# Optimization experiments

Measured on AMD Instinct MI355X. Metric: run time of the kernel, lower is better.

## Reference

```python
import jax, jax.numpy as jnp
import numpy as np
import math

N_EXP = 8
TOP_K = 2
CAPACITY_FACTOR = 1.25


def _capacity(num_tokens):
    cap = math.floor(TOP_K * CAPACITY_FACTOR * num_tokens / N_EXP)
    cap += cap % 2  # round up to even, as in nanoMoE
    return int(cap)


def setup_inputs() -> dict:
    key = jax.random.key(0)
    k1, k2, k3, k4 = jax.random.split(key, 4)
    B, C, d = 4, 1024, 1024
    x = jax.random.normal(k1, (B, C, d), dtype=jnp.float32)
    w_g = jax.random.normal(k2, (d, N_EXP), dtype=jnp.float32) * 0.02
    c_fc = jax.random.normal(k3, (N_EXP, d, 4 * d), dtype=jnp.float32) * 0.02
    c_proj = jax.random.normal(k4, (N_EXP, 4 * d, d), dtype=jnp.float32) * 0.02
    return {"x": x, "w_g": w_g, "c_fc": c_fc, "c_proj": c_proj}


def reference(x, w_g, c_fc, c_proj):
    B, C, d = x.shape
    T = B * C  # num_tokens (static)
    cap = _capacity(T)
    xt = x.reshape(T, d)

    # ---- Router (no noise: use_noisy_top_k=False, eval) ----
    logits = xt @ w_g                                   # [T, n_exp]
    top_v, top_i = jax.lax.top_k(logits, TOP_K)         # [T, k]
    full = jnp.full_like(logits, -jnp.inf)
    full = full.at[jnp.arange(T)[:, None], top_i].set(top_v)
    probs = jax.nn.softmax(full, axis=-1)               # [T, n_exp]

    # expert assignment mask and intra-expert rank (capacity dropping)
    exp_mask = jax.nn.one_hot(top_i, N_EXP, dtype=jnp.int32)       # [T, k, n_exp]
    exp_mask = jnp.transpose(exp_mask, (1, 0, 2))                  # [k, T, n_exp]
    exp_rank = jnp.cumsum(exp_mask.reshape(TOP_K * T, N_EXP), axis=0) - 1
    exp_rank = exp_rank.reshape(TOP_K, T, N_EXP)
    exp_mask = exp_mask * (exp_rank < cap).astype(jnp.int32)       # drop overflow
    exp_rank = jnp.sum(exp_mask * exp_rank, axis=-1)               # [k, T] slot id

    exp_weights = exp_mask.astype(x.dtype) * probs[None]           # [k, T, n_exp]
    rank_oh = jax.nn.one_hot(exp_rank, cap, dtype=x.dtype)         # [k, T, cap]
    # dense combine weights [T, n_exp, cap] (as in original code)
    cb_weight = jnp.einsum('kte,ktc->tec', exp_weights, rank_oh)
    sec_mask = (cb_weight != 0).astype(x.dtype)                    # dispatch mask

    # dispatch tokens into per-expert batches [n_exp, cap, d]
    exp_batches = jnp.einsum('tec,td->ecd', sec_mask, xt)

    # ---- MLPExperts: batched GEMM -> GELU (exact) -> batched GEMM ----
    h = jax.nn.gelu(jnp.einsum('ecd,edf->ecf', exp_batches, c_fc), approximate=False)
    exp_out = jnp.einsum('ecf,efd->ecd', h, c_proj)                # [n_exp, cap, d]

    # ---- weighted combine: [T, n_exp*cap] @ [n_exp*cap, d] ----
    out = cb_weight.reshape(T, N_EXP * cap) @ exp_out.reshape(N_EXP * cap, d)
    return out.reshape(B, C, d)
```

## Files before the change

### kernel.cpp

```cpp
#include <hip/hip_runtime.h>
#include <hip/hip_bf16.h>
#include <math.h>

#define T_TOK 4096
#define D     1024
#define DFF   4096
#define NEXP  8
#define CAP   1280
#define TOPK  2

typedef __bf16 bf16x8 __attribute__((ext_vector_type(8)));
typedef float floatx4 __attribute__((ext_vector_type(4)));

__device__ __forceinline__ unsigned short f2bf(float f) {
  union { float f; unsigned u; } un; un.f = f;
  unsigned r = un.u + 0x7FFF + ((un.u >> 16) & 1);
  return (unsigned short)(r >> 16);
}

__global__ __launch_bounds__(256) void router_kernel(
    const float* __restrict__ x, const float* __restrict__ wg,
    int* __restrict__ top_e, float* __restrict__ top_p) {
  int t = blockIdx.x * 4 + (threadIdx.x >> 6);
  int lane = threadIdx.x & 63;
  if (t >= T_TOK) return;
  const float* xr = x + (size_t)t * D;
  float acc[NEXP];
#pragma unroll
  for (int e = 0; e < NEXP; e++) acc[e] = 0.f;
  for (int dd = lane; dd < D; dd += 64) {
    float xv = xr[dd];
    const float* wr = wg + dd * NEXP;
#pragma unroll
    for (int e = 0; e < NEXP; e++) acc[e] += xv * wr[e];
  }
#pragma unroll
  for (int off = 32; off > 0; off >>= 1) {
#pragma unroll
    for (int e = 0; e < NEXP; e++) acc[e] += __shfl_xor(acc[e], off, 64);
  }
  if (lane == 0) {
    int b0 = 0; float v0 = acc[0];
    for (int e = 1; e < NEXP; e++) if (acc[e] > v0) { v0 = acc[e]; b0 = e; }
    int b1 = -1; float v1 = -INFINITY;
    for (int e = 0; e < NEXP; e++) if (e != b0 && acc[e] > v1) { v1 = acc[e]; b1 = e; }
    float e1 = expf(v1 - v0);
    float s = 1.0f + e1;
    top_e[t * 2 + 0] = b0; top_e[t * 2 + 1] = b1;
    top_p[t * 2 + 0] = 1.0f / s; top_p[t * 2 + 1] = e1 / s;
  }
}

__global__ __launch_bounds__(1024) void rank_kernel(
    const int* __restrict__ top_e, const float* __restrict__ top_p,
    int* __restrict__ slot_token, int* __restrict__ tok_slot,
    float* __restrict__ tok_w) {
  __shared__ int wsum[16][NEXP];
  __shared__ int wscan[16][NEXP];
  int tid = threadIdx.x;
  int lane = tid & 63, w = tid >> 6;

  for (int s = tid; s < NEXP * CAP; s += 1024) slot_token[s] = -1;
  __syncthreads();

  int base[NEXP];
#pragma unroll
  for (int e = 0; e < NEXP; e++) base[e] = 0;

  for (int k = 0; k < TOPK; k++) {
    int cnt[NEXP];
#pragma unroll
    for (int e = 0; e < NEXP; e++) cnt[e] = 0;
    int eloc[4];
#pragma unroll
    for (int i = 0; i < 4; i++) {
      int t = tid * 4 + i;
      int e = top_e[t * 2 + k];
      eloc[i] = e;
#pragma unroll
      for (int q = 0; q < NEXP; q++) cnt[q] += (q == e);
    }
    int inc[NEXP];
#pragma unroll
    for (int e = 0; e < NEXP; e++) inc[e] = cnt[e];
    for (int off = 1; off < 64; off <<= 1) {
#pragma unroll
      for (int e = 0; e < NEXP; e++) {
        int v = __shfl_up(inc[e], off, 64);
        if (lane >= off) inc[e] += v;
      }
    }
    if (lane == 63)
#pragma unroll
      for (int e = 0; e < NEXP; e++) wsum[w][e] = inc[e];
    __syncthreads();
    if (w == 0 && lane < 16) {
      int s[NEXP];
#pragma unroll
      for (int e = 0; e < NEXP; e++) s[e] = wsum[lane][e];
      for (int off = 1; off < 16; off <<= 1) {
#pragma unroll
        for (int e = 0; e < NEXP; e++) {
          int v = __shfl_up(s[e], off, 64);
          if (lane >= off) s[e] += v;
        }
      }
#pragma unroll
      for (int e = 0; e < NEXP; e++) wscan[lane][e] = s[e];
    }
    __syncthreads();
    int excl[NEXP];
#pragma unroll
    for (int e = 0; e < NEXP; e++)
      excl[e] = inc[e] - cnt[e] + (w ? wscan[w - 1][e] : 0) + base[e];

    int run[NEXP];
#pragma unroll
    for (int e = 0; e < NEXP; e++) run[e] = 0;
#pragma unroll
    for (int i = 0; i < 4; i++) {
      int t = tid * 4 + i;
      int e = eloc[i];
      int r = 0;
#pragma unroll
      for (int q = 0; q < NEXP; q++)
        if (q == e) { r = excl[q] + run[q]; run[q]++; }
      if (r < CAP) {
        slot_token[e * CAP + r] = t;
        tok_slot[t * 2 + k] = e * CAP + r;
      } else {
        tok_slot[t * 2 + k] = -1;
      }
      tok_w[t * 2 + k] = top_p[t * 2 + k];
    }
#pragma unroll
    for (int e = 0; e < NEXP; e++) base[e] += wscan[15][e];
    __syncthreads();
  }
}

__global__ __launch_bounds__(256) void gather_cvt_kernel(
    const float* __restrict__ x, const int* __restrict__ slot_token,
    unsigned short* __restrict__ xb) {
  int slot = blockIdx.x;
  int tok = slot_token[slot];
  int i = threadIdx.x;
  float4 v = make_float4(0.f, 0.f, 0.f, 0.f);
  if (tok >= 0) v = ((const float4*)(x + (size_t)tok * D))[i];
  ushort4 o;
  o.x = f2bf(v.x); o.y = f2bf(v.y); o.z = f2bf(v.z); o.w = f2bf(v.w);
  ((ushort4*)(xb + (size_t)slot * D))[i] = o;
}

__global__ __launch_bounds__(256) void transpose_cvt_kernel(
    const float* __restrict__ src, unsigned short* __restrict__ dst,
    int R, int Cc) {
  __shared__ float tile[64][65];
  int e = blockIdx.z;
  src += (size_t)e * R * Cc;
  dst += (size_t)e * R * Cc;
  int r0 = blockIdx.y * 64, c0 = blockIdx.x * 64;
  int tr = threadIdx.x >> 4;
  int tc = (threadIdx.x & 15) * 4;
#pragma unroll
  for (int i = 0; i < 64; i += 16) {
    float4 v = *(const float4*)(src + (size_t)(r0 + tr + i) * Cc + c0 + tc);
    tile[tr + i][tc + 0] = v.x;
    tile[tr + i][tc + 1] = v.y;
    tile[tr + i][tc + 2] = v.z;
    tile[tr + i][tc + 3] = v.w;
  }
  __syncthreads();
#pragma unroll
  for (int i = 0; i < 64; i += 16) {
    int c = tr + i, r = tc;
    ushort4 o;
    o.x = f2bf(tile[r + 0][c]);
    o.y = f2bf(tile[r + 1][c]);
    o.z = f2bf(tile[r + 2][c]);
    o.w = f2bf(tile[r + 3][c]);
    *(ushort4*)(dst + (size_t)(c0 + c) * R + r0 + r) = o;
  }
}

template <int MODE>
__global__ __launch_bounds__(512) void gemm_mfma_kernel(
    const unsigned short* __restrict__ A,
    const unsigned short* __restrict__ Bt,
    void* __restrict__ Cv) {
  constexpr int MM = CAP;
  constexpr int NN = (MODE == 0) ? DFF : D;
  constexpr int LDA = (MODE == 0) ? D : DFF;
  constexpr int KLEN = (MODE == 0) ? D : DFF / 2;

  __shared__ unsigned short As[128 * 32];
  __shared__ unsigned short Bs[128 * 32];

  int e, yt, xt, kh;
  if (MODE == 0) {
    e = blockIdx.x; yt = blockIdx.y; xt = blockIdx.z; kh = 0;
  } else {
    xt = blockIdx.x; yt = blockIdx.y; e = blockIdx.z >> 1; kh = blockIdx.z & 1;
  }

  const unsigned short* Ae = A + (size_t)e * MM * LDA + (size_t)kh * KLEN;
  const unsigned short* Be = Bt + (size_t)e * NN * LDA + (size_t)kh * KLEN;

  int row0 = yt * 128, col0 = xt * 128;
  int tid = threadIdx.x;
  int wave = tid >> 6, lane = tid & 63;

  size_t a_off = (size_t)(row0 + (tid >> 2)) * LDA + (tid & 3) * 8;
  size_t b_off = (size_t)(col0 + (tid >> 2)) * LDA + (tid & 3) * 8;
  unsigned short* as_dst = As + tid * 8;
  unsigned short* bs_dst = Bs + tid * 8;

  int wm = (wave >> 1) * 32;
  int wn = (wave & 1) * 64;
  int fr = lane & 15, fq = lane >> 4;

  floatx4 acc[2][4];
#pragma unroll
  for (int i = 0; i < 2; i++)
#pragma unroll
    for (int j = 0; j < 4; j++) acc[i][j] = (floatx4){0.f, 0.f, 0.f, 0.f};

  for (int k0 = 0; k0 < KLEN; k0 += 32) {
    __builtin_amdgcn_global_load_lds(
        (const __attribute__((address_space(1))) unsigned int*)(Ae + a_off + k0),
        (__attribute__((address_space(3))) unsigned int*)as_dst, 16, 0, 0);
    __builtin_amdgcn_global_load_lds(
        (const __attribute__((address_space(1))) unsigned int*)(Be + b_off + k0),
        (__attribute__((address_space(3))) unsigned int*)bs_dst, 16, 0, 0);
    __syncthreads();

    bf16x8 af[2], bfr[4];
#pragma unroll
    for (int mi = 0; mi < 2; mi++)
      af[mi] = *(const bf16x8*)&As[(wm + mi * 16 + fr) * 32 + fq * 8];
#pragma unroll
    for (int ni = 0; ni < 4; ni++)
      bfr[ni] = *(const bf16x8*)&Bs[(wn + ni * 16 + fr) * 32 + fq * 8];
#pragma unroll
    for (int mi = 0; mi < 2; mi++)
#pragma unroll
      for (int ni = 0; ni < 4; ni++)
        acc[mi][ni] = __builtin_amdgcn_mfma_f32_16x16x32_bf16(
            af[mi], bfr[ni], acc[mi][ni], 0, 0, 0);
    __syncthreads();
  }

  int orow0 = row0 + wm + fq * 4;
  int ocol0 = col0 + wn + fr;
  if (MODE == 0) {
    unsigned short* Cb = (unsigned short*)Cv + (size_t)e * MM * NN;
#pragma unroll
    for (int mi = 0; mi < 2; mi++)
#pragma unroll
      for (int ni = 0; ni < 4; ni++)
#pragma unroll
        for (int r = 0; r < 4; r++) {
          float v = acc[mi][ni][r];
          v = 0.5f * v * (1.f + erff(v * 0.70710678118654752f));
          Cb[(size_t)(orow0 + mi * 16 + r) * NN + (ocol0 + ni * 16)] = f2bf(v);
        }
  } else {
    float* Cf = (float*)Cv + ((size_t)kh * NEXP + e) * MM * NN;
#pragma unroll
    for (int mi = 0; mi < 2; mi++)
#pragma unroll
      for (int ni = 0; ni < 4; ni++)
#pragma unroll
        for (int r = 0; r < 4; r++)
          Cf[(size_t)(orow0 + mi * 16 + r) * NN + (ocol0 + ni * 16)] =
              acc[mi][ni][r];
  }
}

__global__ __launch_bounds__(256) void combine_kernel(
    const float* __restrict__ eo, const int* __restrict__ tok_slot,
    const float* __restrict__ tok_w, float* __restrict__ out) {
  int t = blockIdx.x;
  int i = threadIdx.x;
  const size_t half = (size_t)NEXP * CAP * D;
  float4 acc = make_float4(0.f, 0.f, 0.f, 0.f);
#pragma unroll
  for (int k = 0; k < TOPK; k++) {
    int s = tok_slot[t * 2 + k];
    if (s >= 0) {
      float w = tok_w[t * 2 + k];
      float4 v0 = ((const float4*)(eo + (size_t)s * D))[i];
      float4 v1 = ((const float4*)(eo + half + (size_t)s * D))[i];
      acc.x += w * (v0.x + v1.x);
      acc.y += w * (v0.y + v1.y);
      acc.z += w * (v0.z + v1.z);
      acc.w += w * (v0.w + v1.w);
    }
  }
  ((float4*)(out + (size_t)t * D))[i] = acc;
}

extern "C" void kernel_launch(void* const* d_in, const int* in_sizes, int n_in,
                              void* d_out, int out_size, void* d_ws, size_t ws_size,
                              hipStream_t stream) {
  const float* x     = (const float*)d_in[0];
  const float* wg    = (const float*)d_in[1];
  const float* cfc   = (const float*)d_in[2];
  const float* cproj = (const float*)d_in[3];
  float* out = (float*)d_out;

  char* ws = (char*)d_ws;
  size_t off = 0;
  auto alloc = [&](size_t bytes) -> void* {
    void* p = ws + off;
    off += (bytes + 255) & ~(size_t)255;
    return p;
  };
  int*   top_e      = (int*)  alloc((size_t)T_TOK * 2 * 4);
  float* top_p      = (float*)alloc((size_t)T_TOK * 2 * 4);
  int*   slot_token = (int*)  alloc((size_t)NEXP * CAP * 4);
  int*   tok_slot   = (int*)  alloc((size_t)T_TOK * 2 * 4);
  float* tok_w      = (float*)alloc((size_t)T_TOK * 2 * 4);
  unsigned short* xb      = (unsigned short*)alloc((size_t)NEXP * CAP * D * 2);
  unsigned short* cfc_t   = (unsigned short*)alloc((size_t)NEXP * D * DFF * 2);
  unsigned short* cproj_t = (unsigned short*)alloc((size_t)NEXP * DFF * D * 2);
  unsigned short* h       = (unsigned short*)alloc((size_t)NEXP * CAP * DFF * 2);
  float* eo = (float*)xb;

  transpose_cvt_kernel<<<dim3(DFF / 64, D / 64, NEXP), 256, 0, stream>>>(
      cfc, cfc_t, D, DFF);
  transpose_cvt_kernel<<<dim3(D / 64, DFF / 64, NEXP), 256, 0, stream>>>(
      cproj, cproj_t, DFF, D);

  router_kernel<<<T_TOK / 4, 256, 0, stream>>>(x, wg, top_e, top_p);
  rank_kernel<<<1, 1024, 0, stream>>>(top_e, top_p, slot_token, tok_slot, tok_w);
  gather_cvt_kernel<<<NEXP * CAP, 256, 0, stream>>>(x, slot_token, xb);

  gemm_mfma_kernel<0><<<dim3(NEXP, CAP / 128, DFF / 128), 512, 0, stream>>>(
      xb, cfc_t, h);
  gemm_mfma_kernel<1><<<dim3(D / 128, CAP / 128, NEXP * 2), 512, 0, stream>>>(
      h, cproj_t, eo);

  combine_kernel<<<T_TOK, 256, 0, stream>>>(eo, tok_slot, tok_w, out);
}
```

Measured before the change: 635.5 us.

## Rewrite expert GEMMs with 256x256 tiles, multi-stage LDS pipeline, swizzle

Result: faster. 617.2 us (-2.9%).

```diff
diff --git a/kernel.cpp b/kernel.cpp
--- a/kernel.cpp
+++ b/kernel.cpp
@@ -184,96 +184,173 @@
 }
 
 template <int MODE>
-__global__ __launch_bounds__(512) void gemm_mfma_kernel(
+__global__ __launch_bounds__(512, 2) void gemm8_kernel(
     const unsigned short* __restrict__ A,
     const unsigned short* __restrict__ Bt,
     void* __restrict__ Cv) {
-  constexpr int MM = CAP;
-  constexpr int NN = (MODE == 0) ? DFF : D;
-  constexpr int LDA = (MODE == 0) ? D : DFF;
-  constexpr int KLEN = (MODE == 0) ? D : DFF / 2;
-
-  __shared__ unsigned short As[128 * 32];
-  __shared__ unsigned short Bs[128 * 32];
-
-  int e, yt, xt, kh;
+  constexpr int NN   = (MODE == 0) ? DFF : D;
+  constexpr int KK   = (MODE == 0) ? D : DFF;
+  constexpr int NTN  = NN / 256;
+  constexpr int NKT  = KK / 64;
+  constexpr int STOT = NKT * 4;
+  constexpr int REG  = 256 * 32;
+
+  __shared__ unsigned short As[4 * REG];
+  __shared__ unsigned short Bs[4 * REG];
+
+  int e    = blockIdx.x & 7;
+  int idx  = blockIdx.x >> 3;
+  int row0 = (idx / NTN) * 256;
+  int col0 = (idx % NTN) * 256;
+
+  int tid  = threadIdx.x;
+  int lane = tid & 63, wave = tid >> 6;
+  int wm = wave >> 2, wn = wave & 3;
+  int fr = lane & 15, fq = lane >> 4;
+  int lanesw = (fq ^ ((fr >> 1) & 3)) * 8;
+
+  int srow  = tid >> 2;
+  int lslot = (tid & 3) ^ ((srow >> 1) & 3);
+  const unsigned short* asrc =
+      A + (size_t)e * CAP * KK + (size_t)(row0 + srow) * KK + lslot * 8;
+  const unsigned short* bsrc =
+      Bt + (size_t)e * NN * KK + (size_t)(col0 + srow) * KK + lslot * 8;
+
+  floatx4 acc[8][4];
+#pragma unroll
+  for (int m = 0; m < 8; m++)
+#pragma unroll
+    for (int n = 0; n < 4; n++) acc[m][n] = (floatx4){0.f, 0.f, 0.f, 0.f};
+
+  auto stage = [&](int s) {
+    if (s >= STOT) return;
+    int kt = s >> 2, j = s & 3, hh = j >> 1;
+    const unsigned short* src = (j & 1) ? bsrc : asrc;
+    unsigned short* dst =
+        ((j & 1) ? Bs : As) + ((kt & 1) * 2 + hh) * REG + tid * 8;
+    size_t go = (size_t)kt * 64 + hh * 32;
+    __builtin_amdgcn_global_load_lds(
+        (const __attribute__((address_space(1))) unsigned int*)(src + go),
+        (__attribute__((address_space(3))) unsigned int*)dst, 16, 0, 0);
+    __builtin_amdgcn_global_load_lds(
+        (const __attribute__((address_space(1))) unsigned int*)(src + go +
+                                                               (size_t)128 * KK),
+        (__attribute__((address_space(3))) unsigned int*)(dst + REG / 2), 16, 0,
+        0);
+  };
+
+#pragma unroll
+  for (int s = 0; s < 6; s++) stage(s);
+
+  bf16x8 aq[4], bq[4];
+
+  for (int kt = 0; kt < NKT; kt++) {
+    const unsigned short* a0 = As + (kt & 1) * 2 * REG;
+    const unsigned short* b0 = Bs + (kt & 1) * 2 * REG;
+    const unsigned short* a1 = a0 + REG;
+    const unsigned short* b1 = b0 + REG;
+    int abase = (wm * 128 + fr) * 32 + lanesw;
+    int bbase = (wn * 64 + fr) * 32 + lanesw;
+
+    stage(kt * 4 + 6);
+    if (kt == NKT - 1)
+      asm volatile("s_waitcnt vmcnt(0)" ::: "memory");
+    else
+      asm volatile("s_waitcnt vmcnt(6)" ::: "memory");
+    __builtin_amdgcn_s_barrier();
+    __builtin_amdgcn_sched_barrier(0);
+#pragma unroll
+    for (int n = 0; n < 4; n++)
+      bq[n] = *(const bf16x8*)&b0[bbase + n * 512];
+#pragma unroll
+    for (int m = 0; m < 4; m++)
+      aq[m] = *(const bf16x8*)&a0[abase + m * 512];
+    __builtin_amdgcn_s_setprio(1);
+#pragma unroll
+    for (int m = 0; m < 4; m++)
+#pragma unroll
+      for (int n = 0; n < 4; n++)
+        acc[m][n] = __builtin_amdgcn_mfma_f32_16x16x32_bf16(aq[m], bq[n],
+                                                            acc[m][n], 0, 0, 0);
+    __builtin_amdgcn_s_setprio(0);
+    __builtin_amdgcn_s_barrier();
+
+#pragma unroll
+    for (int m = 0; m < 4; m++)
+      aq[m] = *(const bf16x8*)&a0[abase + 2048 + m * 512];
+    stage(kt * 4 + 7);
+    __builtin_amdgcn_s_barrier();
+    __builtin_amdgcn_s_setprio(1);
+#pragma unroll
+    for (int m = 0; m < 4; m++)
+#pragma unroll
+      for (int n = 0; n < 4; n++)
+        acc[4 + m][n] = __builtin_amdgcn_mfma_f32_16x16x32_bf16(
+            aq[m], bq[n], acc[4 + m][n], 0, 0, 0);
+    __builtin_amdgcn_s_setprio(0);
+    __builtin_amdgcn_s_barrier();
+
+#pragma unroll
+    for (int n = 0; n < 4; n++)
+      bq[n] = *(const bf16x8*)&b1[bbase + n * 512];
+#pragma unroll
+    for (int m = 0; m < 4; m++)
+      aq[m] = *(const bf16x8*)&a1[abase + m * 512];
+    stage(kt * 4 + 8);
+    __builtin_amdgcn_s_barrier();
+    __builtin_amdgcn_s_setprio(1);
+#pragma unroll
+    for (int m = 0; m < 4; m++)
+#pragma unroll
+      for (int n = 0; n < 4; n++)
+        acc[m][n] = __builtin_amdgcn_mfma_f32_16x16x32_bf16(aq[m], bq[n],
+                                                            acc[m][n], 0, 0, 0);
+    __builtin_amdgcn_s_setprio(0);
+    __builtin_amdgcn_s_barrier();
+
+#pragma unroll
+    for (int m = 0; m < 4; m++)
+      aq[m] = *(const bf16x8*)&a1[abase + 2048 + m * 512];
+    stage(kt * 4 + 9);
+    __builtin_amdgcn_s_barrier();
+    __builtin_amdgcn_s_setprio(1);
+#pragma unroll
+    for (int m = 0; m < 4; m++)
+#pragma unroll
+      for (int n = 0; n < 4; n++)
+        acc[4 + m][n] = __builtin_amdgcn_mfma_f32_16x16x32_bf16(
+            aq[m], bq[n], acc[4 + m][n], 0, 0, 0);
+    __builtin_amdgcn_s_setprio(0);
+    __builtin_amdgcn_s_barrier();
+  }
+
   if (MODE == 0) {
-    e = blockIdx.x; yt = blockIdx.y; xt = blockIdx.z; kh = 0;
+    unsigned short* Ce = (unsigned short*)Cv + (size_t)e * CAP * DFF +
+                         (size_t)(row0 + wm * 128 + fq * 4) * DFF + col0 +
+                         wn * 64 + fr;
+#pragma unroll
+    for (int m = 0; m < 8; m++)
+#pragma unroll
+      for (int r = 0; r < 4; r++) {
+        size_t ro = (size_t)(m * 16 + r) * DFF;
+#pragma unroll
+        for (int n = 0; n < 4; n++) {
+          float v = acc[m][n][r];
+          v = 0.5f * v * (1.f + erff(v * 0.70710678118654752f));
+          Ce[ro + n * 16] = f2bf(v);
+        }
+      }
   } else {
-    xt = blockIdx.x; yt = blockIdx.y; e = blockIdx.z >> 1; kh = blockIdx.z & 1;
-  }
-
-  const unsigned short* Ae = A + (size_t)e * MM * LDA + (size_t)kh * KLEN;
-  const unsigned short* Be = Bt + (size_t)e * NN * LDA + (size_t)kh * KLEN;
-
-  int row0 = yt * 128, col0 = xt * 128;
-  int tid = threadIdx.x;
-  int wave = tid >> 6, lane = tid & 63;
-
-  size_t a_off = (size_t)(row0 + (tid >> 2)) * LDA + (tid & 3) * 8;
-  size_t b_off = (size_t)(col0 + (tid >> 2)) * LDA + (tid & 3) * 8;
-  unsigned short* as_dst = As + tid * 8;
-  unsigned short* bs_dst = Bs + tid * 8;
-
-  int wm = (wave >> 1) * 32;
-  int wn = (wave & 1) * 64;
-  int fr = lane & 15, fq = lane >> 4;
-
-  floatx4 acc[2][4];
-#pragma unroll
-  for (int i = 0; i < 2; i++)
-#pragma unroll
-    for (int j = 0; j < 4; j++) acc[i][j] = (floatx4){0.f, 0.f, 0.f, 0.f};
-
-  for (int k0 = 0; k0 < KLEN; k0 += 32) {
-    __builtin_amdgcn_global_load_lds(
-        (const __attribute__((address_space(1))) unsigned int*)(Ae + a_off + k0),
-        (__attribute__((address_space(3))) unsigned int*)as_dst, 16, 0, 0);
-    __builtin_amdgcn_global_load_lds(
-        (const __attribute__((address_space(1))) unsigned int*)(Be + b_off + k0),
-        (__attribute__((address_space(3))) unsigned int*)bs_dst, 16, 0, 0);
-    __syncthreads();
-
-    bf16x8 af[2], bfr[4];
-#pragma unroll
-    for (int mi = 0; mi < 2; mi++)
-      af[mi] = *(const bf16x8*)&As[(wm + mi * 16 + fr) * 32 + fq * 8];
-#pragma unroll
-    for (int ni = 0; ni < 4; ni++)
-      bfr[ni] = *(const bf16x8*)&Bs[(wn + ni * 16 + fr) * 32 + fq * 8];
-#pragma unroll
-    for (int mi = 0; mi < 2; mi++)
-#pragma unroll
-      for (int ni = 0; ni < 4; ni++)
-        acc[mi][ni] = __builtin_amdgcn_mfma_f32_16x16x32_bf16(
-            af[mi], bfr[ni], acc[mi][ni], 0, 0, 0);
-    __syncthreads();
-  }
-
-  int orow0 = row0 + wm + fq * 4;
-  int ocol0 = col0 + wn + fr;
-  if (MODE == 0) {
-    unsigned short* Cb = (unsigned short*)Cv + (size_t)e * MM * NN;
-#pragma unroll
-    for (int mi = 0; mi < 2; mi++)
-#pragma unroll
-      for (int ni = 0; ni < 4; ni++)
-#pragma unroll
-        for (int r = 0; r < 4; r++) {
-          float v = acc[mi][ni][r];
-          v = 0.5f * v * (1.f + erff(v * 0.70710678118654752f));
-          Cb[(size_t)(orow0 + mi * 16 + r) * NN + (ocol0 + ni * 16)] = f2bf(v);
-        }
-  } else {
-    float* Cf = (float*)Cv + ((size_t)kh * NEXP + e) * MM * NN;
-#pragma unroll
-    for (int mi = 0; mi < 2; mi++)
-#pragma unroll
-      for (int ni = 0; ni < 4; ni++)
-#pragma unroll
-        for (int r = 0; r < 4; r++)
-          Cf[(size_t)(orow0 + mi * 16 + r) * NN + (ocol0 + ni * 16)] =
-              acc[mi][ni][r];
+    float* Ce = (float*)Cv + (size_t)e * CAP * D +
+                (size_t)(row0 + wm * 128 + fq * 4) * D + col0 + wn * 64 + fr;
+#pragma unroll
+    for (int m = 0; m < 8; m++)
+#pragma unroll
+      for (int r = 0; r < 4; r++) {
+        size_t ro = (size_t)(m * 16 + r) * D;
+#pragma unroll
+        for (int n = 0; n < 4; n++) Ce[ro + n * 16] = acc[m][n][r];
+      }
   }
 }
 
@@ -282,19 +359,17 @@
     const float* __restrict__ tok_w, float* __restrict__ out) {
   int t = blockIdx.x;
   int i = threadIdx.x;
-  const size_t half = (size_t)NEXP * CAP * D;
   float4 acc = make_float4(0.f, 0.f, 0.f, 0.f);
 #pragma unroll
   for (int k = 0; k < TOPK; k++) {
     int s = tok_slot[t * 2 + k];
     if (s >= 0) {
       float w = tok_w[t * 2 + k];
-      float4 v0 = ((const float4*)(eo + (size_t)s * D))[i];
-      float4 v1 = ((const float4*)(eo + half + (size_t)s * D))[i];
-      acc.x += w * (v0.x + v1.x);
-      acc.y += w * (v0.y + v1.y);
-      acc.z += w * (v0.z + v1.z);
-      acc.w += w * (v0.w + v1.w);
+      float4 v = ((const float4*)(eo + (size_t)s * D))[i];
+      acc.x += w * v.x;
+      acc.y += w * v.y;
+      acc.z += w * v.z;
+      acc.w += w * v.w;
     }
   }
   ((float4*)(out + (size_t)t * D))[i] = acc;
@@ -336,9 +411,9 @@
   rank_kernel<<<1, 1024, 0, stream>>>(top_e, top_p, slot_token, tok_slot, tok_w);
   gather_cvt_kernel<<<NEXP * CAP, 256, 0, stream>>>(x, slot_token, xb);
 
-  gemm_mfma_kernel<0><<<dim3(NEXP, CAP / 128, DFF / 128), 512, 0, stream>>>(
+  gemm8_kernel<0><<<NEXP * (CAP / 256) * (DFF / 256), 512, 0, stream>>>(
       xb, cfc_t, h);
-  gemm_mfma_kernel<1><<<dim3(D / 128, CAP / 128, NEXP * 2), 512, 0, stream>>>(
+  gemm8_kernel<1><<<NEXP * (CAP / 256) * (D / 256), 512, 0, stream>>>(
       h, cproj_t, eo);
 
   combine_kernel<<<T_TOK, 256, 0, stream>>>(eo, tok_slot, tok_w, out);
```
